# Kernel optimization log

Measured on AMD Instinct MI355X. Metric: run time of the kernel, lower is better.

## Reference

```python
import jax, jax.numpy as jnp
import numpy as np

N_NODES = 50000
N_EDGES = 800000
IN_DIM = 128
IN_CH = 64
HIDDEN = 64
OUT_CH = 128
NUM_CLS = 16
NUM_GRAPHS = 512


def setup_inputs() -> dict:
    key = jax.random.key(0)
    ks = jax.random.split(key, 16)
    s = 0.02
    x = jax.random.normal(ks[0], (N_NODES, IN_DIM), jnp.float32)
    edge_index = jax.random.randint(ks[1], (2, N_EDGES), 0, N_NODES, jnp.int64)
    batch = jnp.sort(jax.random.randint(ks[2], (N_NODES,), 0, NUM_GRAPHS, jnp.int64))
    return {
        "x": x,
        "edge_index": edge_index,
        "batch": batch,
        "num_graphs": NUM_GRAPHS,
        "w_stage1": jax.random.normal(ks[3], (IN_DIM, IN_CH), jnp.float32) * s,
        "b_stage1": jnp.zeros((IN_CH,), jnp.float32),
        "rel1_w": jax.random.normal(ks[4], (IN_CH, HIDDEN), jnp.float32) * s,
        "rel1_b": jnp.zeros((HIDDEN,), jnp.float32),
        "root1_w": jax.random.normal(ks[5], (IN_CH, HIDDEN), jnp.float32) * s,
        "rel2_w": jax.random.normal(ks[6], (HIDDEN, 2 * HIDDEN), jnp.float32) * s,
        "rel2_b": jnp.zeros((2 * HIDDEN,), jnp.float32),
        "root2_w": jax.random.normal(ks[7], (HIDDEN, 2 * HIDDEN), jnp.float32) * s,
        "rel3_w": jax.random.normal(ks[8], (2 * HIDDEN, OUT_CH), jnp.float32) * s,
        "rel3_b": jnp.zeros((OUT_CH,), jnp.float32),
        "root3_w": jax.random.normal(ks[9], (2 * HIDDEN, OUT_CH), jnp.float32) * s,
        "lin_w": jax.random.normal(ks[10], (OUT_CH, NUM_CLS), jnp.float32) * s,
        "lin_b": jnp.zeros((NUM_CLS,), jnp.float32),
    }


def graph_conv(x, src, dst, rel_w, rel_b, root_w, n_nodes):
    # PyG GraphConv(aggr='add'): lin_rel(sum_{j in N(i)} x_j) + lin_root(x_i)
    agg = jax.ops.segment_sum(x[src], dst, num_segments=n_nodes)  # [N, in]
    return agg @ rel_w + rel_b + x @ root_w


def reference(x, edge_index, batch, num_graphs,
              w_stage1, b_stage1,
              rel1_w, rel1_b, root1_w,
              rel2_w, rel2_b, root2_w,
              rel3_w, rel3_b, root3_w,
              lin_w, lin_b):
    src, dst = edge_index[0], edge_index[1]
    n = x.shape[0]
    h = x @ w_stage1 + b_stage1                                   # [N, IN_CH]
    h = jax.nn.relu(graph_conv(h, src, dst, rel1_w, rel1_b, root1_w, n))
    h = jax.nn.relu(graph_conv(h, src, dst, rel2_w, rel2_b, root2_w, n))
    h = jax.nn.relu(graph_conv(h, src, dst, rel3_w, rel3_b, root3_w, n))
    # global mean pool over graphs
    sums = jax.ops.segment_sum(h, batch, num_segments=num_graphs)  # [G, OUT_CH]
    cnt = jax.ops.segment_sum(jnp.ones((n,), h.dtype), batch, num_segments=num_graphs)
    pooled = sums / jnp.maximum(cnt, 1.0)[:, None]
    # dropout treated as identity (deterministic eval reference)
    return pooled @ lin_w + lin_b                                  # [G, NUM_CLS]
```

## Files before the change

kernel.cpp:

```cpp
#include <hip/hip_runtime.h>
#include <hip/hip_bf16.h>

#define N_NODES 50000
#define N_EDGES 800000
#define IN_DIM  128
#define IN_CH   64
#define HIDDEN  64
#define OUT_CH  128
#define NUM_CLS 16
#define NUM_G   512
#define NBUK    ((N_NODES + 255) >> 8)
#define BCAP    6144
#define EPB_A   4096
#define S1BLK16 196

typedef __attribute__((ext_vector_type(8))) short short8;
typedef __attribute__((ext_vector_type(4))) float f32x4;

__device__ inline float bits2f(unsigned short u) {
  unsigned x = (unsigned)u << 16;
  float f;
  __builtin_memcpy(&f, &x, 4);
  return f;
}
__device__ inline unsigned short f2bits(float v) {
  __hip_bfloat16 b = __float2bfloat16(v);
  unsigned short s;
  __builtin_memcpy(&s, &b, 2);
  return s;
}
__device__ inline short8 zero8() {
  short8 z;
#pragma unroll
  for (int i = 0; i < 8; ++i) z[i] = 0;
  return z;
}
__device__ inline void acc2(float& a0, float& a1, unsigned v) {
  a0 += bits2f((unsigned short)v);
  a1 += bits2f((unsigned short)(v >> 16));
}
__device__ inline void accu4(float* a, uint4 v) {
  acc2(a[0], a[1], v.x); acc2(a[2], a[3], v.y);
  acc2(a[4], a[5], v.z); acc2(a[6], a[7], v.w);
}

__device__ inline void stage1_wave(const float* __restrict__ Ap,
    const short* __restrict__ Wa, const float* __restrict__ bias,
    unsigned short* __restrict__ outp, int rbase, int lane) {
  constexpr int DIN = 128, DOUT = 64, KT = DIN / 32, CT = DOUT / 16;
  const int m = lane & 15;
  const int q = lane >> 4;
  const int row = rbase + m;
  const bool ok = row < N_NODES;

  short8 afr[KT];
#pragma unroll
  for (int kt = 0; kt < KT; ++kt) {
    short8 f = zero8();
    if (ok) {
      const float* ap = Ap + (size_t)row * DIN + kt * 32 + q * 8;
      float4 x0 = *(const float4*)ap;
      float4 x1 = *(const float4*)(ap + 4);
      f[0] = (short)f2bits(x0.x); f[1] = (short)f2bits(x0.y);
      f[2] = (short)f2bits(x0.z); f[3] = (short)f2bits(x0.w);
      f[4] = (short)f2bits(x1.x); f[5] = (short)f2bits(x1.y);
      f[6] = (short)f2bits(x1.z); f[7] = (short)f2bits(x1.w);
    }
    afr[kt] = f;
  }
#pragma unroll
  for (int ct = 0; ct < CT; ++ct) {
    f32x4 c = {0.f, 0.f, 0.f, 0.f};
#pragma unroll
    for (int kt = 0; kt < KT; ++kt) {
      short8 b = *(const short8*)(Wa + ((size_t)(kt * CT + ct) * 64 + lane) * 8);
      c = __builtin_amdgcn_mfma_f32_16x16x32_bf16(afr[kt], b, c, 0, 0, 0);
    }
    float bv = bias[ct * 16 + m];
#pragma unroll
    for (int r = 0; r < 4; ++r) {
      int ro = rbase + q * 4 + r;
      if (ro < N_NODES) outp[(size_t)ro * DOUT + ct * 16 + m] = f2bits(c[r] + bv);
    }
  }
}

template <int DIN, int DOUT, bool POOL>
__global__ __launch_bounds__(64) void k_fused(
    const unsigned short* __restrict__ h, const int* __restrict__ esrc,
    const int* __restrict__ off, const short* __restrict__ Wa,
    const short* __restrict__ Wh, const float* __restrict__ bias,
    unsigned short* __restrict__ outp, const int* __restrict__ batch,
    float* __restrict__ pooled) {
  constexpr int KT = DIN / 32;
  constexpr int CT = DOUT / 16;
  const int lane = threadIdx.x;
  const int m = lane & 15;
  const int q = lane >> 4;
  const int node = blockIdx.x * 16 + m;

  float acc[KT][8];
#pragma unroll
  for (int kt = 0; kt < KT; ++kt)
#pragma unroll
    for (int j = 0; j < 8; ++j) acc[kt][j] = 0.f;

  {
    int e = off[node], end = off[node + 1];
    const unsigned short* hq = h + q * 8;
    for (; e + 2 <= end; e += 2) {
      int s0 = esrc[e], s1 = esrc[e + 1];
      const unsigned short* r0 = hq + (size_t)s0 * DIN;
      const unsigned short* r1 = hq + (size_t)s1 * DIN;
#pragma unroll
      for (int kt = 0; kt < KT; ++kt) {
        uint4 va = *(const uint4*)(r0 + kt * 32);
        uint4 vb = *(const uint4*)(r1 + kt * 32);
        accu4(acc[kt], va);
        accu4(acc[kt], vb);
      }
    }
    if (e < end) {
      const unsigned short* r0 = hq + (size_t)esrc[e] * DIN;
#pragma unroll
      for (int kt = 0; kt < KT; ++kt)
        accu4(acc[kt], *(const uint4*)(r0 + kt * 32));
    }
  }

  short8 afr[KT], hfr[KT];
#pragma unroll
  for (int kt = 0; kt < KT; ++kt) {
    short8 f;
#pragma unroll
    for (int j = 0; j < 8; ++j) f[j] = (short)f2bits(acc[kt][j]);
    afr[kt] = f;
    hfr[kt] = *(const short8*)(h + (size_t)node * DIN + kt * 32 + q * 8);
  }

  const int rbase = blockIdx.x * 16;

  if constexpr (!POOL) {
#pragma unroll
    for (int ct = 0; ct < CT; ++ct) {
      f32x4 c = {0.f, 0.f, 0.f, 0.f};
#pragma unroll
      for (int kt = 0; kt < KT; ++kt) {
        short8 b = *(const short8*)(Wa + ((size_t)(kt * CT + ct) * 64 + lane) * 8);
        c = __builtin_amdgcn_mfma_f32_16x16x32_bf16(afr[kt], b, c, 0, 0, 0);
        short8 bh = *(const short8*)(Wh + ((size_t)(kt * CT + ct) * 64 + lane) * 8);
        c = __builtin_amdgcn_mfma_f32_16x16x32_bf16(hfr[kt], bh, c, 0, 0, 0);
      }
      float bv = bias[ct * 16 + m];
#pragma unroll
      for (int r = 0; r < 4; ++r) {
        int row = rbase + q * 4 + r;
        outp[(size_t)row * DOUT + ct * 16 + m] = f2bits(fmaxf(c[r] + bv, 0.f));
      }
    }
  } else {
    __shared__ float smem[16][DOUT + 4];
    __shared__ int bsm[16];
    if (lane < 16) bsm[lane] = batch[rbase + lane];
#pragma unroll
    for (int ct = 0; ct < CT; ++ct) {
      f32x4 c = {0.f, 0.f, 0.f, 0.f};
#pragma unroll
      for (int kt = 0; kt < KT; ++kt) {
        short8 b = *(const short8*)(Wa + ((size_t)(kt * CT + ct) * 64 + lane) * 8);
        c = __builtin_amdgcn_mfma_f32_16x16x32_bf16(afr[kt], b, c, 0, 0, 0);
        short8 bh = *(const short8*)(Wh + ((size_t)(kt * CT + ct) * 64 + lane) * 8);
        c = __builtin_amdgcn_mfma_f32_16x16x32_bf16(hfr[kt], bh, c, 0, 0, 0);
      }
      float bv = bias[ct * 16 + m];
#pragma unroll
      for (int r = 0; r < 4; ++r) {
        smem[q * 4 + r][ct * 16 + m] =
            bits2f(f2bits(fmaxf(c[r] + bv, 0.f)));
      }
    }
    __syncthreads();
#pragma unroll
    for (int cc = 0; cc < DOUT / 64; ++cc) {
      const int ch = cc * 64 + lane;
      int g = bsm[0];
      float s = 0.f;
#pragma unroll
      for (int r2 = 0; r2 < 16; ++r2) {
        int gr = bsm[r2];
        if (gr != g) {
          atomicAdd(&pooled[(size_t)g * DOUT + ch], s);
          g = gr;
          s = 0.f;
        }
        s += smem[r2][ch];
      }
      atomicAdd(&pooled[(size_t)g * DOUT + ch], s);
    }
  }
}

template <int DIN, int DOUT>
__device__ inline void pack1(const float* __restrict__ W, short* __restrict__ o,
                             int t) {
  constexpr int CT = DOUT / 16;
  int j = t & 7;
  int lane = (t >> 3) & 63;
  int kc = t >> 9;
  int ct = kc % CT;
  int kt = kc / CT;
  int k = kt * 32 + (lane >> 4) * 8 + j;
  int n = ct * 16 + (lane & 15);
  o[t] = (short)f2bits(W[k * DOUT + n]);
}

struct PackArgs {
  const float *w1, *r1, *o1, *r2, *o2, *r3, *o3;
  short *w1p, *r1p, *o1p, *r2p, *o2p, *r3p, *o3p;
};

__device__ inline void packflat(const PackArgs& a, int t) {
  if      (t < 8192)  pack1<128, 64>(a.w1, a.w1p, t);
  else if (t < 12288) pack1<64, 64>(a.r1, a.r1p, t - 8192);
  else if (t < 16384) pack1<64, 64>(a.o1, a.o1p, t - 12288);
  else if (t < 24576) pack1<64, 128>(a.r2, a.r2p, t - 16384);
  else if (t < 32768) pack1<64, 128>(a.o2, a.o2p, t - 24576);
  else if (t < 49152) pack1<128, 128>(a.r3, a.r3p, t - 32768);
  else if (t < 65536) pack1<128, 128>(a.o3, a.o3p, t - 49152);
}

__global__ __launch_bounds__(256) void k_bucketA(const int* __restrict__ src,
    const int* __restrict__ dst, int* __restrict__ bcnt,
    unsigned* __restrict__ bbuf, float* __restrict__ pooled, PackArgs pk) {
  __shared__ int hist[NBUK], sbase[NBUK], lcur[NBUK], lstart[NBUK];
  __shared__ int sc[256];
  __shared__ unsigned stage[EPB_A];
  __shared__ int s_total;
  const int t = threadIdx.x;

  {
    int g0 = blockIdx.x * 256 + t;
    packflat(pk, g0);
    packflat(pk, g0 + 50176);
    if (g0 < NUM_G * OUT_CH) pooled[g0] = 0.f;
    int g1 = g0 + 50176;
    if (g1 < NUM_G * OUT_CH) pooled[g1] = 0.f;
  }

  for (int i = t; i < NBUK; i += 256) { hist[i] = 0; lcur[i] = 0; }
  __syncthreads();
  const int e0 = blockIdx.x * EPB_A;
  unsigned p_[16];
  int b_[16];
  int cnt = 0;
#pragma unroll
  for (int k = 0; k < 16; ++k) {
    int e = e0 + k * 256 + t;
    if (e < N_EDGES) {
      int sv = src[e], dv = dst[e];
      int bb = dv >> 8;
      p_[cnt] = ((unsigned)bb << 24) | ((unsigned)sv << 8) | ((unsigned)dv & 255u);
      b_[cnt] = bb;
      atomicAdd(&hist[bb], 1);
      cnt++;
    }
  }
  __syncthreads();
  for (int i = t; i < NBUK; i += 256) sbase[i] = atomicAdd(&bcnt[i], hist[i]);
  int hv = (t < NBUK) ? hist[t] : 0;
  sc[t] = hv;
  __syncthreads();
  for (int st = 1; st < 256; st <<= 1) {
    int v = (t >= st) ? sc[t - st] : 0;
    __syncthreads();
    sc[t] += v;
    __syncthreads();
  }
  if (t < NBUK) lstart[t] = sc[t] - hv;
  if (t == 255) s_total = sc[255];
  __syncthreads();
  for (int k = 0; k < cnt; ++k) {
    int bb = b_[k];
    int r = atomicAdd(&lcur[bb], 1);
    stage[lstart[bb] + r] = p_[k];
  }
  __syncthreads();
  const int total = s_total;
  for (int j = t; j < total; j += 256) {
    unsigned v = stage[j];
    int bb = (int)(v >> 24);
    int gpos = sbase[bb] + (j - lstart[bb]);
    if (gpos < BCAP) bbuf[(size_t)bb * BCAP + gpos] = v & 0x00FFFFFFu;
  }
}

__global__ __launch_bounds__(1024) void k_bfin_s1(const int* __restrict__ bcnt,
    const unsigned* __restrict__ bbuf, int* __restrict__ off,
    int* __restrict__ esrc,
    const float* __restrict__ x, const short* __restrict__ w1p,
    const float* __restrict__ b1, unsigned short* __restrict__ P) {
  if (blockIdx.x >= NBUK) {
    const int bs = blockIdx.x - NBUK;
    const int wave = threadIdx.x >> 6;
    const int lane = threadIdx.x & 63;
    stage1_wave(x, w1p, b1, P, bs * 256 + wave * 16, lane);
    return;
  }

  __shared__ int cnt2[4096];
  __shared__ int s[256];
  __shared__ int bbase_s;
  const int b = blockIdx.x;
  const int t = threadIdx.x;
  const int nt = 1024;

  for (int i = t; i < 4096; i += nt) cnt2[i] = 0;

  int bv0 = (t < NBUK) ? min(bcnt[t], BCAP) : 0;
  if (t < 256) s[t] = bv0;
  __syncthreads();
  for (int st = 1; st < 256; st <<= 1) {
    int v = (t >= st && t < 256) ? s[t - st] : 0;
    __syncthreads();
    if (t < 256) s[t] += v;
    __syncthreads();
  }
  if (t == b) bbase_s = s[t] - bv0;
  if (b == 0 && t == NBUK - 1) off[N_NODES] = s[t];
  __syncthreads();
  const int bb = bbase_s;

  const int n = min(bcnt[b], BCAP);
  for (int i = t; i < n; i += nt) {
    unsigned p = bbuf[(size_t)b * BCAP + i];
    int key = (int)(p & 255u) * 16 + (int)((p >> 8) >> 12);
    atomicAdd(&cnt2[key], 1);
  }
  __syncthreads();

  int v0 = 0;
  if (t < 256) {
    int run = 0;
#pragma unroll
    for (int i = 0; i < 16; ++i) {
      int tmp = cnt2[t * 16 + i];
      cnt2[t * 16 + i] = run;
      run += tmp;
    }
    v0 = run;
    s[t] = v0;
  }
  __syncthreads();
  for (int st = 1; st < 256; st <<= 1) {
    int v = (t >= st && t < 256) ? s[t - st] : 0;
    __syncthreads();
    if (t < 256) s[t] += v;
    __syncthreads();
  }
  if (t < 256) {
    const int myoff = bb + s[t] - v0;
    const int node = b * 256 + t;
    if (node < N_NODES) off[node] = myoff;
#pragma unroll
    for (int i = 0; i < 16; ++i) cnt2[t * 16 + i] += myoff;
  }
  __syncthreads();

  for (int i = t; i < n; i += nt) {
    unsigned p = bbuf[(size_t)b * BCAP + i];
    int srcv = (int)(p >> 8);
    int key = (int)(p & 255u) * 16 + (srcv >> 12);
    int pos = atomicAdd(&cnt2[key], 1);
    esrc[pos] = srcv;
  }
}

__device__ inline int lbound(const int* __restrict__ a, int n, int v) {
  int lo = 0, hi = n;
  while (lo < hi) {
    int m = (lo + hi) >> 1;
    if (a[m] < v) lo = m + 1; else hi = m;
  }
  return lo;
}

__global__ __launch_bounds__(128) void k_head(const float* __restrict__ pooled,
    const int* __restrict__ batch, const float* __restrict__ lw,
    const float* __restrict__ lb, float* __restrict__ out) {
  __shared__ float sp[128];
  int g = blockIdx.x;
  int t = threadIdx.x;
  int lo = lbound(batch, N_NODES, g);
  int hi = lbound(batch, N_NODES, g + 1);
  float inv = (hi > lo) ? 1.f / (float)(hi - lo) : 0.f;
  sp[t] = pooled[(size_t)g * OUT_CH + t] * inv;
  __syncthreads();
  if (t < NUM_CLS) {
    float s = lb[t];
#pragma unroll
    for (int k = 0; k < OUT_CH; ++k) s = fmaf(sp[k], lw[k * NUM_CLS + t], s);
    out[g * NUM_CLS + t] = s;
  }
}

extern "C" void kernel_launch(void* const* d_in, const int* in_sizes, int n_in,
                              void* d_out, int out_size, void* d_ws, size_t ws_size,
                              hipStream_t stream) {
  const float* x      = (const float*)d_in[0];
  const int*   ei     = (const int*)d_in[1];
  const int*   batch  = (const int*)d_in[2];
  const float* w1     = (const float*)d_in[4];
  const float* b1     = (const float*)d_in[5];
  const float* rel1w  = (const float*)d_in[6];
  const float* rel1b  = (const float*)d_in[7];
  const float* root1w = (const float*)d_in[8];
  const float* rel2w  = (const float*)d_in[9];
  const float* rel2b  = (const float*)d_in[10];
  const float* root2w = (const float*)d_in[11];
  const float* rel3w  = (const float*)d_in[12];
  const float* rel3b  = (const float*)d_in[13];
  const float* root3w = (const float*)d_in[14];
  const float* linw   = (const float*)d_in[15];
  const float* linb   = (const float*)d_in[16];
  const int* src = ei;
  const int* dst = ei + N_EDGES;
  float* out = (float*)d_out;

  unsigned short* P = (unsigned short*)d_ws;
  unsigned short* Q = P + (size_t)N_NODES * 128;
  unsigned short* R = Q + (size_t)N_NODES * 128;
  short* WP = (short*)(R + (size_t)N_NODES * 128);
  short* w1p  = WP;
  short* r1p  = w1p + 8192;
  short* o1p  = r1p + 4096;
  short* r2p  = o1p + 4096;
  short* o2p  = r2p + 8192;
  short* r3p  = o2p + 8192;
  short* o3p  = r3p + 16384;
  int* off     = (int*)(o3p + 16384);
  int* bcnt    = off + (N_NODES + 1);
  float* pooled = (float*)(bcnt + NBUK);
  int* esrc    = (int*)(pooled + NUM_G * OUT_CH) + 3;
  unsigned* bbuf = (unsigned*)(esrc + N_EDGES);

  PackArgs pk = {w1, rel1w, root1w, rel2w, root2w, rel3w, root3w,
                 w1p, r1p, o1p, r2p, o2p, r3p, o3p};

  hipMemsetAsync(bcnt, 0, NBUK * sizeof(int), stream);
  k_bucketA<<<(N_EDGES + EPB_A - 1) / EPB_A, 256, 0, stream>>>(src, dst, bcnt,
                                                               bbuf, pooled, pk);
  k_bfin_s1<<<NBUK + S1BLK16, 1024, 0, stream>>>(bcnt, bbuf, off, esrc,
                                                 x, w1p, b1, P);

  const int GF = (N_NODES + 15) / 16;

  k_fused<64, 64, false><<<GF, 64, 0, stream>>>(P, esrc, off, r1p, o1p, rel1b,
                                                R, batch, pooled);
  k_fused<64, 128, false><<<GF, 64, 0, stream>>>(R, esrc, off, r2p, o2p, rel2b,
                                                 Q, batch, pooled);
  k_fused<128, 128, true><<<GF, 64, 0, stream>>>(Q, esrc, off, r3p, o3p, rel3b,
                                                 P, batch, pooled);
  k_head<<<NUM_G, 128, 0, stream>>>(pooled, batch, linw, linb, out);
}
```

Before: 229.2 us.

## Double-buffer neighbor row gathers into LDS via async global_load_lds for DIN=64

For the 64-wide GraphConv layers, neighbor feature rows are gathered with global_load_lds into a double-buffered LDS staging area, four edges per step, with explicit vmcnt waits. The next batch's source indices are loaded while the current batch is in flight. The aim is to hide gather latency by keeping more memory requests outstanding. In exchange the loop runs to the maximum degree among the 16 nodes in a wave, so low-degree lanes issue wasted clamped loads. It also relies on a hand-counted vmcnt value and uses more LDS.

```diff
diff --git a/kernel.cpp b/kernel.cpp
--- a/kernel.cpp
+++ b/kernel.cpp
@@ -105,7 +105,71 @@
 #pragma unroll
     for (int j = 0; j < 8; ++j) acc[kt][j] = 0.f;
 
-  {
+  if constexpr (DIN == 64) {
+    __shared__ uint4 lbuf[2][4][KT][64];
+    const int offv = off[node];
+    const int end = off[node + 1];
+    const int deg = end - offv;
+    int mx = deg;
+#pragma unroll
+    for (int d = 1; d < 16; d <<= 1) mx = max(mx, __shfl_xor(mx, d));
+    const int nb = (mx + 3) >> 2;
+
+    const unsigned short* hq = h + q * 8;
+
+    auto ldix = [&](int k, int (&ix)[4]) {
+#pragma unroll
+      for (int j = 0; j < 4; ++j) {
+        int e = offv + k * 4 + j;
+        int ec = (e < end) ? e : ((deg > 0) ? end - 1 : 0);
+        ix[j] = esrc[ec];
+      }
+    };
+    auto issue = [&](int k, const int (&ix)[4]) {
+#pragma unroll
+      for (int j = 0; j < 4; ++j)
+#pragma unroll
+        for (int kt = 0; kt < KT; ++kt) {
+          const unsigned short* g = hq + (size_t)ix[j] * DIN + kt * 32;
+          __builtin_amdgcn_global_load_lds((const unsigned int*)g,
+                                           (unsigned int*)&lbuf[k & 1][j][kt][0],
+                                           16, 0, 0);
+        }
+    };
+    auto procb = [&](int k) {
+#pragma unroll
+      for (int j = 0; j < 4; ++j) {
+        if (offv + k * 4 + j < end) {
+#pragma unroll
+          for (int kt = 0; kt < KT; ++kt) {
+            uint4 v = lbuf[k & 1][j][kt][lane];
+            accu4(acc[kt], v);
+          }
+        }
+      }
+    };
+
+    if (nb > 0) {
+      int ixA[4], ixB[4];
+      ldix(0, ixA);
+      issue(0, ixA);
+      ldix(1, ixB);
+      for (int k = 1; k < nb; ++k) {
+        issue(k, ixB);
+        ldix(k + 1, ixA);
+        asm volatile("s_waitcnt vmcnt(16)" ::: "memory");
+        __builtin_amdgcn_sched_barrier(0);
+        procb(k - 1);
+#pragma unroll
+        for (int j2 = 0; j2 < 4; ++j2) {
+          int t0 = ixA[j2]; ixA[j2] = ixB[j2]; ixB[j2] = t0;
+        }
+      }
+      asm volatile("s_waitcnt vmcnt(0)" ::: "memory");
+      __builtin_amdgcn_sched_barrier(0);
+      procb(nb - 1);
+    }
+  } else {
     int e = off[node], end = off[node + 1];
     const unsigned short* hq = h + q * 8;
     for (; e + 2 <= end; e += 2) {
```

New measurement: 253.1 us. +10.4%, slower.
